# Optimization experiments

Hardware: AMD Instinct MI355X
Metric: run time of the kernel (lower is better)

The kernel has to match this reference:

```python
import jax, jax.numpy as jnp
import numpy as np

B, T, D, H, S = 512, 256, 128, 128, 32


def _param(key, shape, scale):
    return (jax.random.normal(key, shape, dtype=jnp.float32) * scale)


def setup_inputs() -> dict:
    key = jax.random.key(0)
    ks = jax.random.split(key, 32)
    sD = 1.0 / np.sqrt(D)
    sH = 1.0 / np.sqrt(H)
    inp = {
        'x': jax.random.normal(ks[0], (B, T, D), dtype=jnp.float32),
        'statics': jax.random.normal(ks[1], (B, S), dtype=jnp.float32),
        'mask': (jax.random.uniform(ks[2], (B, T, D)) > 0.5).astype(jnp.float32),
        'delta': jax.random.uniform(ks[3], (B, T, D), dtype=jnp.float32),
        'x_last_observed': jax.random.normal(ks[4], (B, T, D), dtype=jnp.float32),
        'x_mean': jax.random.normal(ks[5], (B, D), dtype=jnp.float32),
        'hs0': jax.random.normal(ks[6], (B, H), dtype=jnp.float32),
        # GRU-D decay params
        'w_dg_x': _param(ks[7], (D,), sD), 'b_dg_x': jnp.zeros((D,), jnp.float32),
        'W_dg_h': _param(ks[8], (H, D), sD), 'b_dg_h': jnp.zeros((H,), jnp.float32),
        # gates: update z, reset r, candidate h
        'W_z': _param(ks[9], (H, D), sD), 'U_z': _param(ks[10], (H, H), sH),
        'V_z': _param(ks[11], (H, D), sD), 'b_z': jnp.zeros((H,), jnp.float32),
        'W_r': _param(ks[12], (H, D), sD), 'U_r': _param(ks[13], (H, H), sH),
        'V_r': _param(ks[14], (H, D), sD), 'b_r': jnp.zeros((H,), jnp.float32),
        'W_h': _param(ks[15], (H, D), sD), 'U_h': _param(ks[16], (H, H), sH),
        'V_h': _param(ks[17], (H, D), sD), 'b_h': jnp.zeros((H,), jnp.float32),
        # classifier
        'W_out': _param(ks[18], (1, H + S), 1.0 / np.sqrt(H + S)),
        'b_out': jnp.zeros((1,), jnp.float32),
    }
    return inp


def reference(x, statics, mask, delta, x_last_observed, x_mean, hs0,
              w_dg_x, b_dg_x, W_dg_h, b_dg_h,
              W_z, U_z, V_z, b_z, W_r, U_r, V_r, b_r,
              W_h, U_h, V_h, b_h, W_out, b_out):
    # scan over time: inputs [T, B, D]
    xs = jnp.transpose(x, (1, 0, 2))
    ms = jnp.transpose(mask, (1, 0, 2))
    ds = jnp.transpose(delta, (1, 0, 2))
    xl = jnp.transpose(x_last_observed, (1, 0, 2))

    def step(h, inputs):
        xv, m, d, xlast = inputs
        gamma_x = jnp.exp(-jax.nn.relu(w_dg_x * d + b_dg_x))            # [B, D]
        gamma_h = jnp.exp(-jax.nn.relu(d @ W_dg_h.T + b_dg_h))          # [B, H]
        x_hat = m * xv + (1.0 - m) * (gamma_x * xlast + (1.0 - gamma_x) * x_mean)
        h = gamma_h * h
        z = jax.nn.sigmoid(x_hat @ W_z.T + h @ U_z.T + m @ V_z.T + b_z)
        r = jax.nn.sigmoid(x_hat @ W_r.T + h @ U_r.T + m @ V_r.T + b_r)
        h_tilde = jnp.tanh(x_hat @ W_h.T + (r * h) @ U_h.T + m @ V_h.T + b_h)
        h = (1.0 - z) * h + z * h_tilde
        return h, None

    h_final, _ = jax.lax.scan(step, hs0, (xs, ms, ds, xl))
    full = jnp.concatenate([h_final, statics], axis=1)                  # [B, H+S]
    predictions = full @ W_out.T + b_out                                # [B, 1]
    return predictions
```

## Files before the change

### kernel.cpp

```cpp
#include <hip/hip_runtime.h>
#include <stdint.h>


#define B_ 512
#define T_ 256
#define D_ 128
#define H_ 128
#define S_ 32
#define NE 512
#define KA 384
#define M_ (B_*T_)
#define HP 136
#define ESLAB ((size_t)NE * 16)
#define ESTRIDE ((size_t)32 * ESLAB)

typedef __attribute__((ext_vector_type(8))) short short8;
typedef __attribute__((ext_vector_type(4))) float f32x4;

#define BAR_LDS() asm volatile("s_waitcnt lgkmcnt(0)\n\ts_barrier" ::: "memory")

__device__ __forceinline__ unsigned short f2bf(float f) {
  union { float f; uint32_t u; } v; v.f = f;
  return (unsigned short)((v.u + 0x7FFFu + ((v.u >> 16) & 1u)) >> 16);
}
__device__ __forceinline__ unsigned short f2bf_fast(float f) {
  union { float f; uint32_t u; } v; v.f = f;
  return (unsigned short)((v.u + 0x8000u) >> 16);
}
__device__ __forceinline__ float bf2f(uint32_t s) {
  union { uint32_t u; float f; } v; v.u = s << 16;
  return v.f;
}

__device__ __forceinline__ uint2  ldraw(const unsigned short* p) { return *(const uint2*)p; }
__device__ __forceinline__ float4 ldraw(const float* p)          { return *(const float4*)p; }
__device__ __forceinline__ void unp(uint2 v, float o[4]) {
  o[0] = bf2f(v.x & 0xffffu); o[1] = bf2f(v.x >> 16);
  o[2] = bf2f(v.y & 0xffffu); o[3] = bf2f(v.y >> 16);
}
__device__ __forceinline__ void unp(float4 v, float o[4]) {
  o[0] = v.x; o[1] = v.y; o[2] = v.z; o[3] = v.w;
}
__device__ __forceinline__ void st4(unsigned short* p, const float v[4]) {
  uint2 u;
  u.x = (uint32_t)f2bf(v[0]) | ((uint32_t)f2bf(v[1]) << 16);
  u.y = (uint32_t)f2bf(v[2]) | ((uint32_t)f2bf(v[3]) << 16);
  *(uint2*)p = u;
}
__device__ __forceinline__ void st4(float* p, const float v[4]) {
  *(float4*)p = make_float4(v[0], v[1], v[2], v[3]);
}

__device__ __forceinline__ float fsigmoid(float x) {
  return __builtin_amdgcn_rcpf(1.f + __expf(-x));
}
__device__ __forceinline__ float ftanh(float x) {
  return 1.f - 2.f * __builtin_amdgcn_rcpf(1.f + __expf(2.f * x));
}

#define ASYNC_CP16(gsrc, ldst) \
  __builtin_amdgcn_global_load_lds((const __attribute__((address_space(1))) void*)(gsrc), \
                                   (__attribute__((address_space(3))) void*)(ldst), 16, 0, 0)

__global__ void prep_weights(const float* __restrict__ Wz, const float* __restrict__ Vz,
                             const float* __restrict__ Wr, const float* __restrict__ Vr,
                             const float* __restrict__ Wh, const float* __restrict__ Vh,
                             const float* __restrict__ Wdgh,
                             const float* __restrict__ bz, const float* __restrict__ br,
                             const float* __restrict__ bh, const float* __restrict__ bdgh,
                             unsigned short* __restrict__ Wcat, float* __restrict__ bias)
{
  int id = blockIdx.x * 256 + threadIdx.x;
  if (id < NE * KA) {
    int n = id / KA, k = id - n * KA;
    float v = 0.f;
    if (n < 384) {
      int nn = n & 127;
      const float* W = (n < 128) ? Wz : (n < 256) ? Wr : Wh;
      const float* V = (n < 128) ? Vz : (n < 256) ? Vr : Vh;
      if (k < 128)      v = W[nn * 128 + k];
      else if (k < 256) v = V[nn * 128 + (k - 128)];
    } else {
      if (k >= 256) v = Wdgh[(n - 384) * 128 + (k - 256)];
    }
    Wcat[id] = f2bf(v);
  }
  if (id < NE) {
    bias[id] = (id < 128) ? bz[id] : (id < 256) ? br[id - 128]
             : (id < 384) ? bh[id - 256] : bdgh[id - 384];
  }
}

__global__ void build_A(const float* __restrict__ x, const float* __restrict__ mask,
                        const float* __restrict__ delta, const float* __restrict__ xlast,
                        const float* __restrict__ xmean,
                        const float* __restrict__ wdgx, const float* __restrict__ bdgx,
                        unsigned short* __restrict__ Abuf)
{
  int id = blockIdx.x * 256 + threadIdx.x;
  int m = id >> 5;
  int c = id & 31;
  int t = m >> 9;
  int b = m & (B_ - 1);
  int k = c * 4;
  size_t src = ((size_t)b * T_ + t) * D_ + k;
  float4 xv = *(const float4*)(x + src);
  float4 mv = *(const float4*)(mask + src);
  float4 dv = *(const float4*)(delta + src);
  float4 lv = *(const float4*)(xlast + src);
  float4 uv = *(const float4*)(xmean + (size_t)b * D_ + k);
  float4 wv = *(const float4*)(wdgx + k);
  float4 bv = *(const float4*)(bdgx + k);
  const float* xp = (const float*)&xv; const float* mp = (const float*)&mv;
  const float* dp = (const float*)&dv; const float* lp = (const float*)&lv;
  const float* up = (const float*)&uv; const float* wp = (const float*)&wv;
  const float* bp = (const float*)&bv;
  unsigned short xh[4], mm[4], dd[4];
  #pragma unroll
  for (int i = 0; i < 4; ++i) {
    float g = __expf(-fmaxf(wp[i] * dp[i] + bp[i], 0.f));
    float xhat = mp[i] * xp[i] + (1.f - mp[i]) * (g * lp[i] + (1.f - g) * up[i]);
    xh[i] = f2bf(xhat); mm[i] = f2bf(mp[i]); dd[i] = f2bf(dp[i]);
  }
  uint2 px, pm, pd;
  px.x = (uint32_t)xh[0] | ((uint32_t)xh[1] << 16); px.y = (uint32_t)xh[2] | ((uint32_t)xh[3] << 16);
  pm.x = (uint32_t)mm[0] | ((uint32_t)mm[1] << 16); pm.y = (uint32_t)mm[2] | ((uint32_t)mm[3] << 16);
  pd.x = (uint32_t)dd[0] | ((uint32_t)dd[1] << 16); pd.y = (uint32_t)dd[2] | ((uint32_t)dd[3] << 16);
  unsigned short* rowp = Abuf + (size_t)m * KA;
  *(uint2*)(rowp + k)       = px;
  *(uint2*)(rowp + 128 + k) = pm;
  *(uint2*)(rowp + 256 + k) = pd;
}

template <typename ET>
__global__ __launch_bounds__(256, 2) void gemm_phase1(
    const unsigned short* __restrict__ Abuf, const unsigned short* __restrict__ Wcat,
    const float* __restrict__ bias, ET* __restrict__ E)
{
  __shared__ unsigned short As[3][4096];
  __shared__ unsigned short Bs[3][4096];
  const int tid = threadIdx.x;
  const int wave = tid >> 6, lane = tid & 63;
  const int q = lane >> 4, rl = lane & 15;
  const int m0 = blockIdx.x * 128;
  const int n0 = blockIdx.y * 128;
  const int wm = (wave >> 1) * 64, wn = (wave & 1) * 64;

  f32x4 acc[4][4];
  #pragma unroll
  for (int a = 0; a < 4; ++a)
    #pragma unroll
    for (int b = 0; b < 4; ++b) acc[a][b] = (f32x4){0.f, 0.f, 0.f, 0.f};

  #define STAGE(kt_) do {                                                     \
    const int kbase_ = (kt_) * 32; const int buf_ = (kt_) % 3;                \
    _Pragma("unroll")                                                         \
    for (int i = 0; i < 2; ++i) {                                             \
      int chunk = i * 256 + wave * 64 + lane;                                 \
      int row = chunk >> 2, kc = chunk & 3;                                   \
      ASYNC_CP16(Abuf + (size_t)(m0 + row) * KA + kbase_ + kc * 8,            \
                 &As[buf_][(i * 256 + wave * 64) * 8]);                       \
      ASYNC_CP16(Wcat + (size_t)(n0 + row) * KA + kbase_ + kc * 8,            \
                 &Bs[buf_][(i * 256 + wave * 64) * 8]);                       \
    }                                                                         \
  } while (0)

  STAGE(0);
  STAGE(1);

  #pragma unroll
  for (int kt = 0; kt < 12; ++kt) {
    if (kt == 11) asm volatile("s_waitcnt vmcnt(0)" ::: "memory");
    else          asm volatile("s_waitcnt vmcnt(4)" ::: "memory");
    asm volatile("s_barrier" ::: "memory");
    if (kt < 10) STAGE(kt + 2);
    const int buf = kt % 3;
    short8 af[4], bfr[4];
    #pragma unroll
    for (int tm = 0; tm < 4; ++tm)
      af[tm] = *(const short8*)(&As[buf][(wm + tm * 16 + rl) * 32 + q * 8]);
    #pragma unroll
    for (int tn = 0; tn < 4; ++tn)
      bfr[tn] = *(const short8*)(&Bs[buf][(wn + tn * 16 + rl) * 32 + q * 8]);
    #pragma unroll
    for (int tm = 0; tm < 4; ++tm)
      #pragma unroll
      for (int tn = 0; tn < 4; ++tn)
        acc[tm][tn] = __builtin_amdgcn_mfma_f32_16x16x32_bf16(af[tm], bfr[tn], acc[tm][tn], 0, 0, 0);
  }
  #undef STAGE

  const int t = m0 >> 9;
  const int bbase = m0 & (B_ - 1);
  #pragma unroll
  for (int tn = 0; tn < 4; ++tn) {
    int n = n0 + wn + tn * 16 + rl;
    float bv = bias[n];
    bool isg = (n >= 384);
    #pragma unroll
    for (int tm = 0; tm < 4; ++tm) {
      int brow = bbase + wm + tm * 16;
      float v[4];
      #pragma unroll
      for (int reg = 0; reg < 4; ++reg) {
        float xv = acc[tm][tn][reg] + bv;
        v[reg] = isg ? __expf(-fmaxf(xv, 0.f)) : xv;
      }
      st4(E + ((size_t)t * 32 + (brow >> 4)) * ESLAB + (size_t)n * 16 + q * 4, v);
    }
  }
}

template <typename ET>
__global__ __launch_bounds__(512, 2) void grud_scan(
    const ET* __restrict__ E,
    const float* __restrict__ Uz, const float* __restrict__ Ur, const float* __restrict__ Uh,
    const float* __restrict__ hs0, const float* __restrict__ statics,
    const float* __restrict__ Wout, const float* __restrict__ bout,
    float* __restrict__ out)
{
  __shared__ unsigned short hdec[16 * HP];
  __shared__ unsigned short rhb[16 * HP];
  __shared__ float hfin[16 * HP];
  const int tid = threadIdx.x;
  const int wave = tid >> 6, lane = tid & 63;
  const int q = lane >> 4, rl = lane & 15;
  const int col = wave * 16 + rl;
  const int b0 = blockIdx.x * 16;

  short8 uz[4], ur[4], uh[4];
  #pragma unroll
  for (int kc = 0; kc < 4; ++kc) {
    int koff = kc * 32 + q * 8;
    const float* pzw = Uz + col * H_ + koff;
    const float* prw = Ur + col * H_ + koff;
    const float* phw = Uh + col * H_ + koff;
    #pragma unroll
    for (int j = 0; j < 8; ++j) {
      uz[kc][j] = (short)f2bf(pzw[j]);
      ur[kc][j] = (short)f2bf(prw[j]);
      uh[kc][j] = (short)f2bf(phw[j]);
    }
  }

  const ET* pz = E + (size_t)blockIdx.x * ESLAB + (size_t)col * 16 + q * 4;
  const ET* pr = pz + 128 * 16;
  const ET* ph = pz + 256 * 16;
  const ET* pg = pz + 384 * 16;

  using RawT = decltype(ldraw((const ET*)nullptr));
  RawT cz, cr, chh, cg, nz{}, nr{}, nh{}, ng{};
  cz  = ldraw(pz);
  cr  = ldraw(pr);
  chh = ldraw(ph);
  cg  = ldraw(pg + ESTRIDE);
  RawT g0raw = ldraw(pg);

  float hd[4], g0[4];
  unp(g0raw, g0);
  #pragma unroll
  for (int reg = 0; reg < 4; ++reg) {
    int row = q * 4 + reg;
    float h0 = hs0[(b0 + row) * H_ + col];
    hd[reg] = g0[reg] * h0;
    hdec[row * HP + col] = f2bf_fast(hd[reg]);
  }
  BAR_LDS();

  for (int t = 0; t < T_; ++t) {
    if (t + 1 < T_) {
      size_t off = (size_t)(t + 1) * ESTRIDE;
      nz = ldraw(pz + off); nr = ldraw(pr + off); nh = ldraw(ph + off);
      if (t + 2 < T_) ng = ldraw(pg + (size_t)(t + 2) * ESTRIDE);
    }
    float Pz[4], Pr[4], Ph[4];
    unp(cz, Pz); unp(cr, Pr); unp(chh, Ph);

    short8 af[4];
    #pragma unroll
    for (int kc = 0; kc < 4; ++kc)
      af[kc] = *(const short8*)(&hdec[rl * HP + kc * 32 + q * 8]);
    f32x4 accz = (f32x4){0.f,0.f,0.f,0.f}, accr = (f32x4){0.f,0.f,0.f,0.f};
    #pragma unroll
    for (int kc = 0; kc < 4; ++kc) {
      accz = __builtin_amdgcn_mfma_f32_16x16x32_bf16(af[kc], uz[kc], accz, 0, 0, 0);
      accr = __builtin_amdgcn_mfma_f32_16x16x32_bf16(af[kc], ur[kc], accr, 0, 0, 0);
    }
    float zz[4];
    #pragma unroll
    for (int reg = 0; reg < 4; ++reg) {
      zz[reg] = fsigmoid(accz[reg] + Pz[reg]);
      float rr = fsigmoid(accr[reg] + Pr[reg]);
      rhb[(q * 4 + reg) * HP + col] = f2bf_fast(rr * hd[reg]);
    }
    BAR_LDS();

    short8 ar[4];
    #pragma unroll
    for (int kc = 0; kc < 4; ++kc)
      ar[kc] = *(const short8*)(&rhb[rl * HP + kc * 32 + q * 8]);
    f32x4 acch = (f32x4){0.f,0.f,0.f,0.f};
    #pragma unroll
    for (int kc = 0; kc < 4; ++kc)
      acch = __builtin_amdgcn_mfma_f32_16x16x32_bf16(ar[kc], uh[kc], acch, 0, 0, 0);

    if (t < T_ - 1) {
      float Gn[4];
      unp(cg, Gn);
      #pragma unroll
      for (int reg = 0; reg < 4; ++reg) {
        float ht = ftanh(acch[reg] + Ph[reg]);
        float hn = hd[reg] + zz[reg] * (ht - hd[reg]);
        hd[reg] = Gn[reg] * hn;
        hdec[(q * 4 + reg) * HP + col] = f2bf_fast(hd[reg]);
      }
    } else {
      #pragma unroll
      for (int reg = 0; reg < 4; ++reg) {
        float ht = ftanh(acch[reg] + Ph[reg]);
        float hn = hd[reg] + zz[reg] * (ht - hd[reg]);
        hfin[(q * 4 + reg) * HP + col] = hn;
      }
    }
    BAR_LDS();

    cz = nz; cr = nr; chh = nh; cg = ng;
  }

  {
    int row = tid >> 5, j = tid & 31;
    float acc = 0.f;
    #pragma unroll
    for (int c0 = 0; c0 < 4; ++c0)
      acc += hfin[row * HP + j + c0 * 32] * Wout[j + c0 * 32];
    acc += statics[(size_t)(b0 + row) * S_ + j] * Wout[H_ + j];
    #pragma unroll
    for (int off = 16; off >= 1; off >>= 1)
      acc += __shfl_down(acc, off, 32);
    if (j == 0) out[b0 + row] = acc + bout[0];
  }
}

template <typename ET>
static void launch_all(void* const* d_in, float* out, char* ws, hipStream_t stream)
{
  const float* x      = (const float*)d_in[0];
  const float* statics= (const float*)d_in[1];
  const float* mask   = (const float*)d_in[2];
  const float* delta  = (const float*)d_in[3];
  const float* xlast  = (const float*)d_in[4];
  const float* xmean  = (const float*)d_in[5];
  const float* hs0    = (const float*)d_in[6];
  const float* wdgx   = (const float*)d_in[7];
  const float* bdgx   = (const float*)d_in[8];
  const float* Wdgh   = (const float*)d_in[9];
  const float* bdgh   = (const float*)d_in[10];
  const float* Wz     = (const float*)d_in[11];
  const float* Uz     = (const float*)d_in[12];
  const float* Vz     = (const float*)d_in[13];
  const float* bz     = (const float*)d_in[14];
  const float* Wr     = (const float*)d_in[15];
  const float* Ur     = (const float*)d_in[16];
  const float* Vr     = (const float*)d_in[17];
  const float* br     = (const float*)d_in[18];
  const float* Wh     = (const float*)d_in[19];
  const float* Uh     = (const float*)d_in[20];
  const float* Vh     = (const float*)d_in[21];
  const float* bh     = (const float*)d_in[22];
  const float* Wout   = (const float*)d_in[23];
  const float* bout   = (const float*)d_in[24];

  const size_t eBytes = (size_t)M_ * NE * sizeof(ET);
  const size_t aBytes = (size_t)M_ * KA * 2;
  const size_t wBytes = (size_t)NE * KA * 2;
  ET* E = (ET*)ws;
  unsigned short* Abuf = (unsigned short*)(ws + eBytes);
  unsigned short* Wcat = (unsigned short*)(ws + eBytes + aBytes);
  float* bias = (float*)(ws + eBytes + aBytes + wBytes);

  prep_weights<<<768, 256, 0, stream>>>(Wz, Vz, Wr, Vr, Wh, Vh, Wdgh,
                                        bz, br, bh, bdgh, Wcat, bias);
  build_A<<<(M_ * 32) / 256, 256, 0, stream>>>(x, mask, delta, xlast, xmean,
                                               wdgx, bdgx, Abuf);
  gemm_phase1<ET><<<dim3(M_ / 128, NE / 128), 256, 0, stream>>>(Abuf, Wcat, bias, E);
  grud_scan<ET><<<B_ / 16, 512, 0, stream>>>(E, Uz, Ur, Uh, hs0, statics, Wout, bout, out);
}

extern "C" void kernel_launch(void* const* d_in, const int* in_sizes, int n_in,
                              void* d_out, int out_size, void* d_ws, size_t ws_size,
                              hipStream_t stream)
{
  char* ws = (char*)d_ws;
  float* out = (float*)d_out;
  const size_t common = (size_t)M_ * KA * 2 + (size_t)NE * KA * 2 + 8192;
  const size_t needF32 = (size_t)M_ * NE * 4 + common;
  const size_t needBF  = (size_t)M_ * NE * 2 + common;
  if (ws_size >= needF32)     launch_all<float>(d_in, out, ws, stream);
  else if (ws_size >= needBF) launch_all<unsigned short>(d_in, out, ws, stream);
}
```

Before: 605.4 us.

## Halve scan block to 4 waves, each computing two 16-column tiles

The recurrent scan kernel now runs 256 threads (4 waves) per batch tile instead of 512. Each wave handles two 16-column output tiles, so it holds twice the U-weight fragments in registers and reuses each loaded A fragment across two MFMAs. The aim is cheaper barriers and fewer LDS fragment reads per timestep on the serial critical path. The cost is more register pressure and more serial work per wave, with only 32 blocks in the grid and less latency hiding.

```diff
diff --git a/kernel.cpp b/kernel.cpp
--- a/kernel.cpp
+++ b/kernel.cpp
@@ -212,7 +212,7 @@
 }
 
 template <typename ET>
-__global__ __launch_bounds__(512, 2) void grud_scan(
+__global__ __launch_bounds__(256, 1) void grud_scan(
     const ET* __restrict__ E,
     const float* __restrict__ Uz, const float* __restrict__ Ur, const float* __restrict__ Uh,
     const float* __restrict__ hs0, const float* __restrict__ statics,
@@ -225,73 +225,94 @@
   const int tid = threadIdx.x;
   const int wave = tid >> 6, lane = tid & 63;
   const int q = lane >> 4, rl = lane & 15;
-  const int col = wave * 16 + rl;
   const int b0 = blockIdx.x * 16;
 
-  short8 uz[4], ur[4], uh[4];
-  #pragma unroll
-  for (int kc = 0; kc < 4; ++kc) {
-    int koff = kc * 32 + q * 8;
-    const float* pzw = Uz + col * H_ + koff;
-    const float* prw = Ur + col * H_ + koff;
-    const float* phw = Uh + col * H_ + koff;
-    #pragma unroll
-    for (int j = 0; j < 8; ++j) {
-      uz[kc][j] = (short)f2bf(pzw[j]);
-      ur[kc][j] = (short)f2bf(prw[j]);
-      uh[kc][j] = (short)f2bf(phw[j]);
-    }
-  }
-
-  const ET* pz = E + (size_t)blockIdx.x * ESLAB + (size_t)col * 16 + q * 4;
-  const ET* pr = pz + 128 * 16;
-  const ET* ph = pz + 256 * 16;
-  const ET* pg = pz + 384 * 16;
+  int col[2];
+  col[0] = wave * 32 + rl;
+  col[1] = col[0] + 16;
+
+  short8 uz[2][4], ur[2][4], uh[2][4];
+  #pragma unroll
+  for (int c = 0; c < 2; ++c) {
+    #pragma unroll
+    for (int kc = 0; kc < 4; ++kc) {
+      int koff = kc * 32 + q * 8;
+      const float* pzw = Uz + col[c] * H_ + koff;
+      const float* prw = Ur + col[c] * H_ + koff;
+      const float* phw = Uh + col[c] * H_ + koff;
+      #pragma unroll
+      for (int j = 0; j < 8; ++j) {
+        uz[c][kc][j] = (short)f2bf(pzw[j]);
+        ur[c][kc][j] = (short)f2bf(prw[j]);
+        uh[c][kc][j] = (short)f2bf(phw[j]);
+      }
+    }
+  }
+
+  const ET* pz[2];
+  pz[0] = E + (size_t)blockIdx.x * ESLAB + (size_t)col[0] * 16 + q * 4;
+  pz[1] = pz[0] + 16 * 16;
 
   using RawT = decltype(ldraw((const ET*)nullptr));
-  RawT cz, cr, chh, cg, nz{}, nr{}, nh{}, ng{};
-  cz  = ldraw(pz);
-  cr  = ldraw(pr);
-  chh = ldraw(ph);
-  cg  = ldraw(pg + ESTRIDE);
-  RawT g0raw = ldraw(pg);
-
-  float hd[4], g0[4];
-  unp(g0raw, g0);
-  #pragma unroll
-  for (int reg = 0; reg < 4; ++reg) {
-    int row = q * 4 + reg;
-    float h0 = hs0[(b0 + row) * H_ + col];
-    hd[reg] = g0[reg] * h0;
-    hdec[row * HP + col] = f2bf_fast(hd[reg]);
+  RawT cz[2], cr[2], chh[2], cg[2], nz[2], nr[2], nh[2], ng[2];
+  float hd[2][4];
+  #pragma unroll
+  for (int c = 0; c < 2; ++c) {
+    cz[c]  = ldraw(pz[c]);
+    cr[c]  = ldraw(pz[c] + 128 * 16);
+    chh[c] = ldraw(pz[c] + 256 * 16);
+    cg[c]  = ldraw(pz[c] + 384 * 16 + ESTRIDE);
+    RawT g0raw = ldraw(pz[c] + 384 * 16);
+    float g0[4]; unp(g0raw, g0);
+    #pragma unroll
+    for (int reg = 0; reg < 4; ++reg) {
+      int row = q * 4 + reg;
+      float h0 = hs0[(b0 + row) * H_ + col[c]];
+      hd[c][reg] = g0[reg] * h0;
+      hdec[row * HP + col[c]] = f2bf_fast(hd[c][reg]);
+    }
+    nz[c] = cz[c]; nr[c] = cr[c]; nh[c] = chh[c]; ng[c] = cg[c];
   }
   BAR_LDS();
 
   for (int t = 0; t < T_; ++t) {
     if (t + 1 < T_) {
       size_t off = (size_t)(t + 1) * ESTRIDE;
-      nz = ldraw(pz + off); nr = ldraw(pr + off); nh = ldraw(ph + off);
-      if (t + 2 < T_) ng = ldraw(pg + (size_t)(t + 2) * ESTRIDE);
-    }
-    float Pz[4], Pr[4], Ph[4];
-    unp(cz, Pz); unp(cr, Pr); unp(chh, Ph);
+      #pragma unroll
+      for (int c = 0; c < 2; ++c) {
+        nz[c] = ldraw(pz[c] + off);
+        nr[c] = ldraw(pz[c] + 128 * 16 + off);
+        nh[c] = ldraw(pz[c] + 256 * 16 + off);
+        if (t + 2 < T_) ng[c] = ldraw(pz[c] + 384 * 16 + off + ESTRIDE);
+      }
+    }
 
     short8 af[4];
     #pragma unroll
     for (int kc = 0; kc < 4; ++kc)
       af[kc] = *(const short8*)(&hdec[rl * HP + kc * 32 + q * 8]);
-    f32x4 accz = (f32x4){0.f,0.f,0.f,0.f}, accr = (f32x4){0.f,0.f,0.f,0.f};
+    f32x4 accz[2], accr[2];
+    accz[0] = (f32x4){0.f,0.f,0.f,0.f}; accz[1] = (f32x4){0.f,0.f,0.f,0.f};
+    accr[0] = (f32x4){0.f,0.f,0.f,0.f}; accr[1] = (f32x4){0.f,0.f,0.f,0.f};
     #pragma unroll
     for (int kc = 0; kc < 4; ++kc) {
-      accz = __builtin_amdgcn_mfma_f32_16x16x32_bf16(af[kc], uz[kc], accz, 0, 0, 0);
-      accr = __builtin_amdgcn_mfma_f32_16x16x32_bf16(af[kc], ur[kc], accr, 0, 0, 0);
-    }
-    float zz[4];
-    #pragma unroll
-    for (int reg = 0; reg < 4; ++reg) {
-      zz[reg] = fsigmoid(accz[reg] + Pz[reg]);
-      float rr = fsigmoid(accr[reg] + Pr[reg]);
-      rhb[(q * 4 + reg) * HP + col] = f2bf_fast(rr * hd[reg]);
+      #pragma unroll
+      for (int c = 0; c < 2; ++c) {
+        accz[c] = __builtin_amdgcn_mfma_f32_16x16x32_bf16(af[kc], uz[c][kc], accz[c], 0, 0, 0);
+        accr[c] = __builtin_amdgcn_mfma_f32_16x16x32_bf16(af[kc], ur[c][kc], accr[c], 0, 0, 0);
+      }
+    }
+    float zz[2][4];
+    #pragma unroll
+    for (int c = 0; c < 2; ++c) {
+      float Pz[4], Pr[4];
+      unp(cz[c], Pz); unp(cr[c], Pr);
+      #pragma unroll
+      for (int reg = 0; reg < 4; ++reg) {
+        zz[c][reg] = fsigmoid(accz[c][reg] + Pz[reg]);
+        float rr = fsigmoid(accr[c][reg] + Pr[reg]);
+        rhb[(q * 4 + reg) * HP + col[c]] = f2bf_fast(rr * hd[c][reg]);
+      }
     }
     BAR_LDS();
 
@@ -299,45 +320,63 @@
     #pragma unroll
     for (int kc = 0; kc < 4; ++kc)
       ar[kc] = *(const short8*)(&rhb[rl * HP + kc * 32 + q * 8]);
-    f32x4 acch = (f32x4){0.f,0.f,0.f,0.f};
+    f32x4 acch[2];
+    acch[0] = (f32x4){0.f,0.f,0.f,0.f}; acch[1] = (f32x4){0.f,0.f,0.f,0.f};
     #pragma unroll
     for (int kc = 0; kc < 4; ++kc)
-      acch = __builtin_amdgcn_mfma_f32_16x16x32_bf16(ar[kc], uh[kc], acch, 0, 0, 0);
+      #pragma unroll
+      for (int c = 0; c < 2; ++c)
+        acch[c] = __builtin_amdgcn_mfma_f32_16x16x32_bf16(ar[kc], uh[c][kc], acch[c], 0, 0, 0);
 
     if (t < T_ - 1) {
-      float Gn[4];
-      unp(cg, Gn);
-      #pragma unroll
-      for (int reg = 0; reg < 4; ++reg) {
-        float ht = ftanh(acch[reg] + Ph[reg]);
-        float hn = hd[reg] + zz[reg] * (ht - hd[reg]);
-        hd[reg] = Gn[reg] * hn;
-        hdec[(q * 4 + reg) * HP + col] = f2bf_fast(hd[reg]);
+      #pragma unroll
+      for (int c = 0; c < 2; ++c) {
+        float Ph[4], Gn[4];
+        unp(chh[c], Ph); unp(cg[c], Gn);
+        #pragma unroll
+        for (int reg = 0; reg < 4; ++reg) {
+          float ht = ftanh(acch[c][reg] + Ph[reg]);
+          float hn = hd[c][reg] + zz[c][reg] * (ht - hd[c][reg]);
+          hd[c][reg] = Gn[reg] * hn;
+          hdec[(q * 4 + reg) * HP + col[c]] = f2bf_fast(hd[c][reg]);
+        }
       }
     } else {
       #pragma unroll
-      for (int reg = 0; reg < 4; ++reg) {
-        float ht = ftanh(acch[reg] + Ph[reg]);
-        float hn = hd[reg] + zz[reg] * (ht - hd[reg]);
-        hfin[(q * 4 + reg) * HP + col] = hn;
+      for (int c = 0; c < 2; ++c) {
+        float Ph[4];
+        unp(chh[c], Ph);
+        #pragma unroll
+        for (int reg = 0; reg < 4; ++reg) {
+          float ht = ftanh(acch[c][reg] + Ph[reg]);
+          float hn = hd[c][reg] + zz[c][reg] * (ht - hd[c][reg]);
+          hfin[(q * 4 + reg) * HP + col[c]] = hn;
+        }
       }
     }
     BAR_LDS();
 
-    cz = nz; cr = nr; chh = nh; cg = ng;
+    #pragma unroll
+    for (int c = 0; c < 2; ++c) {
+      cz[c] = nz[c]; cr[c] = nr[c]; chh[c] = nh[c]; cg[c] = ng[c];
+    }
   }
 
   {
-    int row = tid >> 5, j = tid & 31;
-    float acc = 0.f;
-    #pragma unroll
-    for (int c0 = 0; c0 < 4; ++c0)
-      acc += hfin[row * HP + j + c0 * 32] * Wout[j + c0 * 32];
-    acc += statics[(size_t)(b0 + row) * S_ + j] * Wout[H_ + j];
-    #pragma unroll
-    for (int off = 16; off >= 1; off >>= 1)
-      acc += __shfl_down(acc, off, 32);
-    if (j == 0) out[b0 + row] = acc + bout[0];
+    int j = tid & 31;
+    #pragma unroll
+    for (int r0 = 0; r0 < 16; r0 += 8) {
+      int row = r0 + (tid >> 5);
+      float acc = 0.f;
+      #pragma unroll
+      for (int c0 = 0; c0 < 4; ++c0)
+        acc += hfin[row * HP + j + c0 * 32] * Wout[j + c0 * 32];
+      acc += statics[(size_t)(b0 + row) * S_ + j] * Wout[H_ + j];
+      #pragma unroll
+      for (int off = 16; off >= 1; off >>= 1)
+        acc += __shfl_down(acc, off, 32);
+      if (j == 0) out[b0 + row] = acc + bout[0];
+    }
   }
 }
 
@@ -383,7 +422,7 @@
   build_A<<<(M_ * 32) / 256, 256, 0, stream>>>(x, mask, delta, xlast, xmean,
                                                wdgx, bdgx, Abuf);
   gemm_phase1<ET><<<dim3(M_ / 128, NE / 128), 256, 0, stream>>>(Abuf, Wcat, bias, E);
-  grud_scan<ET><<<B_ / 16, 512, 0, stream>>>(E, Uz, Ur, Uh, hs0, statics, Wout, bout, out);
+  grud_scan<ET><<<B_ / 16, 256, 0, stream>>>(E, Uz, Ur, Uh, hs0, statics, Wout, bout, out);
 }
 
 extern "C" void kernel_launch(void* const* d_in, const int* in_sizes, int n_in,
```

Result: slower. 683.1 us (+12.8%).

## Swizzle LDS hidden-state layout and unroll scan by two with split MFMA chains

Applied to the files above, without the earlier changes.

Stores the hidden state and r*h in shared memory in a fragment-native swizzled layout, so each lane reads its MFMA operand as one contiguous 8-element vector. The recurrent loop is unrolled by two with ping-pong prefetch registers, which removes the per-step register copies. Each gate's dot product is split into two independent MFMA accumulator chains so the dependent-MFMA latency is shorter. The z-sigmoid is moved after the barrier so it overlaps the r*h reads. The aim is to cut the latency of the serial 256-step chain, at the cost of more registers and more complex indexing.

```diff
diff --git a/kernel.cpp b/kernel.cpp
--- a/kernel.cpp
+++ b/kernel.cpp
@@ -219,8 +219,8 @@
     const float* __restrict__ Wout, const float* __restrict__ bout,
     float* __restrict__ out)
 {
-  __shared__ unsigned short hdec[16 * HP];
-  __shared__ unsigned short rhb[16 * HP];
+  __shared__ unsigned short hdec[2048];
+  __shared__ unsigned short rhb[2048];
   __shared__ float hfin[16 * HP];
   const int tid = threadIdx.x;
   const int wave = tid >> 6, lane = tid & 63;
@@ -228,6 +228,9 @@
   const int col = wave * 16 + rl;
   const int b0 = blockIdx.x * 16;
 
+  const int wbase = (col >> 5) * 512 + ((col >> 3) & 3) * 128 + q * 32 + (col & 7);
+  const int rdbase = lane * 8;
+
   short8 uz[4], ur[4], uh[4];
   #pragma unroll
   for (int kc = 0; kc < 4; ++kc) {
@@ -249,11 +252,11 @@
   const ET* pg = pz + 384 * 16;
 
   using RawT = decltype(ldraw((const ET*)nullptr));
-  RawT cz, cr, chh, cg, nz{}, nr{}, nh{}, ng{};
-  cz  = ldraw(pz);
-  cr  = ldraw(pr);
-  chh = ldraw(ph);
-  cg  = ldraw(pg + ESTRIDE);
+  RawT cz0, cr0, ch0, cg0, cz1, cr1, ch1, cg1;
+  cz0 = ldraw(pz);
+  cr0 = ldraw(pr);
+  ch0 = ldraw(ph);
+  cg0 = ldraw(pg + ESTRIDE);
   RawT g0raw = ldraw(pg);
 
   float hd[4], g0[4];
@@ -263,69 +266,92 @@
     int row = q * 4 + reg;
     float h0 = hs0[(b0 + row) * H_ + col];
     hd[reg] = g0[reg] * h0;
-    hdec[row * HP + col] = f2bf_fast(hd[reg]);
+    hdec[wbase + reg * 8] = f2bf_fast(hd[reg]);
   }
   BAR_LDS();
 
-  for (int t = 0; t < T_; ++t) {
-    if (t + 1 < T_) {
-      size_t off = (size_t)(t + 1) * ESTRIDE;
-      nz = ldraw(pz + off); nr = ldraw(pr + off); nh = ldraw(ph + off);
-      if (t + 2 < T_) ng = ldraw(pg + (size_t)(t + 2) * ESTRIDE);
-    }
-    float Pz[4], Pr[4], Ph[4];
-    unp(cz, Pz); unp(cr, Pr); unp(chh, Ph);
-
-    short8 af[4];
-    #pragma unroll
-    for (int kc = 0; kc < 4; ++kc)
-      af[kc] = *(const short8*)(&hdec[rl * HP + kc * 32 + q * 8]);
-    f32x4 accz = (f32x4){0.f,0.f,0.f,0.f}, accr = (f32x4){0.f,0.f,0.f,0.f};
-    #pragma unroll
-    for (int kc = 0; kc < 4; ++kc) {
-      accz = __builtin_amdgcn_mfma_f32_16x16x32_bf16(af[kc], uz[kc], accz, 0, 0, 0);
-      accr = __builtin_amdgcn_mfma_f32_16x16x32_bf16(af[kc], ur[kc], accr, 0, 0, 0);
-    }
-    float zz[4];
-    #pragma unroll
-    for (int reg = 0; reg < 4; ++reg) {
-      zz[reg] = fsigmoid(accz[reg] + Pz[reg]);
-      float rr = fsigmoid(accr[reg] + Pr[reg]);
-      rhb[(q * 4 + reg) * HP + col] = f2bf_fast(rr * hd[reg]);
-    }
-    BAR_LDS();
-
-    short8 ar[4];
-    #pragma unroll
-    for (int kc = 0; kc < 4; ++kc)
-      ar[kc] = *(const short8*)(&rhb[rl * HP + kc * 32 + q * 8]);
-    f32x4 acch = (f32x4){0.f,0.f,0.f,0.f};
-    #pragma unroll
-    for (int kc = 0; kc < 4; ++kc)
-      acch = __builtin_amdgcn_mfma_f32_16x16x32_bf16(ar[kc], uh[kc], acch, 0, 0, 0);
-
-    if (t < T_ - 1) {
-      float Gn[4];
-      unp(cg, Gn);
-      #pragma unroll
-      for (int reg = 0; reg < 4; ++reg) {
-        float ht = ftanh(acch[reg] + Ph[reg]);
-        float hn = hd[reg] + zz[reg] * (ht - hd[reg]);
-        hd[reg] = Gn[reg] * hn;
-        hdec[(q * 4 + reg) * HP + col] = f2bf_fast(hd[reg]);
-      }
-    } else {
-      #pragma unroll
-      for (int reg = 0; reg < 4; ++reg) {
-        float ht = ftanh(acch[reg] + Ph[reg]);
-        float hn = hd[reg] + zz[reg] * (ht - hd[reg]);
-        hfin[(q * 4 + reg) * HP + col] = hn;
-      }
-    }
-    BAR_LDS();
-
-    cz = nz; cr = nr; chh = nh; cg = ng;
-  }
+  #define STEP(CZ, CR, CH, CG, NZ, NR, NH, NG, T_IDX) do {                    \
+    const int t = (T_IDX);                                                    \
+                                  \
+    short8 af[4];                                                             \
+    _Pragma("unroll")                                                         \
+    for (int kc = 0; kc < 4; ++kc)                                            \
+      af[kc] = *(const short8*)(&hdec[kc * 512 + rdbase]);                    \
+                   \
+    if (t + 1 < T_) {                                                         \
+      size_t off = (size_t)(t + 1) * ESTRIDE;                                 \
+      NZ = ldraw(pz + off); NR = ldraw(pr + off); NH = ldraw(ph + off);       \
+      if (t + 2 < T_) NG = ldraw(pg + off + ESTRIDE);                         \
+    }                                                                         \
+                                     \
+    f32x4 za = (f32x4){0.f,0.f,0.f,0.f}, zb = (f32x4){0.f,0.f,0.f,0.f};       \
+    f32x4 ra = (f32x4){0.f,0.f,0.f,0.f}, rb = (f32x4){0.f,0.f,0.f,0.f};       \
+    za = __builtin_amdgcn_mfma_f32_16x16x32_bf16(af[0], uz[0], za, 0, 0, 0);  \
+    ra = __builtin_amdgcn_mfma_f32_16x16x32_bf16(af[0], ur[0], ra, 0, 0, 0);  \
+    zb = __builtin_amdgcn_mfma_f32_16x16x32_bf16(af[2], uz[2], zb, 0, 0, 0);  \
+    rb = __builtin_amdgcn_mfma_f32_16x16x32_bf16(af[2], ur[2], rb, 0, 0, 0);  \
+    za = __builtin_amdgcn_mfma_f32_16x16x32_bf16(af[1], uz[1], za, 0, 0, 0);  \
+    ra = __builtin_amdgcn_mfma_f32_16x16x32_bf16(af[1], ur[1], ra, 0, 0, 0);  \
+    zb = __builtin_amdgcn_mfma_f32_16x16x32_bf16(af[3], uz[3], zb, 0, 0, 0);  \
+    rb = __builtin_amdgcn_mfma_f32_16x16x32_bf16(af[3], ur[3], rb, 0, 0, 0);  \
+                    \
+    {                                                                         \
+      float Pr[4]; unp(CR, Pr);                                               \
+      f32x4 rs = ra + rb;                                                     \
+      _Pragma("unroll")                                                       \
+      for (int reg = 0; reg < 4; ++reg) {                                     \
+        float rr = fsigmoid(rs[reg] + Pr[reg]);                               \
+        rhb[wbase + reg * 8] = f2bf_fast(rr * hd[reg]);                       \
+      }                                                                       \
+    }                                                                         \
+    BAR_LDS();                                                 \
+                      \
+    short8 ar[4];                                                             \
+    _Pragma("unroll")                                                         \
+    for (int kc = 0; kc < 4; ++kc)                                            \
+      ar[kc] = *(const short8*)(&rhb[kc * 512 + rdbase]);                     \
+    float zz[4];                                                              \
+    {                                                                         \
+      float Pz[4]; unp(CZ, Pz);                                               \
+      f32x4 zs = za + zb;                                                     \
+      _Pragma("unroll")                                                       \
+      for (int reg = 0; reg < 4; ++reg)                                       \
+        zz[reg] = fsigmoid(zs[reg] + Pz[reg]);                                \
+    }                                                                         \
+    f32x4 ha = (f32x4){0.f,0.f,0.f,0.f}, hb = (f32x4){0.f,0.f,0.f,0.f};       \
+    ha = __builtin_amdgcn_mfma_f32_16x16x32_bf16(ar[0], uh[0], ha, 0, 0, 0);  \
+    hb = __builtin_amdgcn_mfma_f32_16x16x32_bf16(ar[2], uh[2], hb, 0, 0, 0);  \
+    ha = __builtin_amdgcn_mfma_f32_16x16x32_bf16(ar[1], uh[1], ha, 0, 0, 0);  \
+    hb = __builtin_amdgcn_mfma_f32_16x16x32_bf16(ar[3], uh[3], hb, 0, 0, 0);  \
+    {                                                                         \
+      f32x4 hs = ha + hb;                                                     \
+      float Ph[4]; unp(CH, Ph);                                               \
+      if (t < T_ - 1) {                                                       \
+        float Gn[4]; unp(CG, Gn);                                             \
+        _Pragma("unroll")                                                     \
+        for (int reg = 0; reg < 4; ++reg) {                                   \
+          float ht = ftanh(hs[reg] + Ph[reg]);                                \
+          float hn = hd[reg] + zz[reg] * (ht - hd[reg]);     \
+          hd[reg] = Gn[reg] * hn;                             \
+          hdec[wbase + reg * 8] = f2bf_fast(hd[reg]);                         \
+        }                                                                     \
+      } else {                                                                \
+        _Pragma("unroll")                                                     \
+        for (int reg = 0; reg < 4; ++reg) {                                   \
+          float ht = ftanh(hs[reg] + Ph[reg]);                                \
+          float hn = hd[reg] + zz[reg] * (ht - hd[reg]);                      \
+          hfin[(q * 4 + reg) * HP + col] = hn;                                \
+        }                                                                     \
+      }                                                                       \
+    }                                                                         \
+    BAR_LDS();                                                 \
+  } while (0)
+
+  for (int th = 0; th < T_ / 2; ++th) {
+    STEP(cz0, cr0, ch0, cg0, cz1, cr1, ch1, cg1, 2 * th);
+    STEP(cz1, cr1, ch1, cg1, cz0, cr0, ch0, cg0, 2 * th + 1);
+  }
+  #undef STEP
 
   {
     int row = tid >> 5, j = tid & 31;
```

New measurement: 608.6 us. Within noise of the previous version (+0.5%).
